# Kernel tuning notes

Hardware: AMD Instinct MI355X
Metric: run time of the kernel (lower is better)

Reference implementation:

```python
import jax, jax.numpy as jnp
import numpy as np

N, NUM_ST, NUM_LT = 8, 256, 4096
C_ST, C_LT, C_LAT = 512, 512, 128
LN_EPS = 1e-3  # keras LayerNormalization default epsilon


def setup_inputs() -> dict:
    key = jax.random.key(0)
    ks = jax.random.split(key, 12)
    w = lambda k, shape, sc=0.05: jax.random.normal(k, shape, jnp.float32) * sc
    return {
        "st_feat": jax.random.normal(ks[0], (N, NUM_ST, 1, 1, C_ST), jnp.float32),
        "lt_feat": jax.random.normal(ks[1], (N, NUM_LT, 1, 1, C_LT), jnp.float32),
        # conv1x1 kernels stored as (in, out) matrices
        "w_st": w(ks[2], (C_ST, C_LAT)),
        "b_st": w(ks[3], (C_LAT,), 0.01),
        "w_lt": w(ks[4], (C_LT, C_LAT)),
        "b_lt": w(ks[5], (C_LAT,), 0.01),
        "w_g": w(ks[6], (C_LT, C_LAT)),
        "b_g": w(ks[7], (C_LAT,), 0.01),
        # LayerNorm over axes [1,2,3,4] of (n, C_LAT, NUM_ST, 1, 1)
        "ln_gamma": 1.0 + w(ks[8], (C_LAT, NUM_ST, 1, 1), 0.02),
        "ln_beta": w(ks[9], (C_LAT, NUM_ST, 1, 1), 0.02),
        # out_conv: Conv3D on tensor with last dim 1 -> in_channels=1, kernel (out,)
        "w_out": w(ks[10], (C_ST,)),
        "b_out": w(ks[11], (C_ST,), 0.01),
    }


def reference(st_feat, lt_feat, w_st, b_st, w_lt, b_lt, w_g, b_g,
              ln_gamma, ln_beta, w_out, b_out):
    n = st_feat.shape[0]
    # 1x1x1 conv projections == matmul over last (channel) dim
    theta = jnp.einsum('nshwc,cd->nshwd', st_feat, w_st) + b_st  # (n,S,1,1,c)
    phi = jnp.einsum('nlhwc,cd->nlhwd', lt_feat, w_lt) + b_lt    # (n,L,1,1,c)
    g = jnp.einsum('nlhwc,cd->nlhwd', lt_feat, w_g) + b_g        # (n,L,1,1,c)
    # Faithful raw reshapes (row-major reinterpretation, as in the TF code)
    theta = theta.reshape(n, C_LAT, NUM_ST)
    phi = phi.reshape(n, C_LAT, NUM_LT)
    g = g.reshape(n, C_LAT, NUM_LT)
    # theta^T @ phi  -> (n, S, L)
    attn = jnp.einsum('ncs,ncl->nsl', theta, phi)
    attn = attn / jnp.sqrt(jnp.asarray(C_LAT, jnp.float32))  # use_scale
    p = jax.nn.softmax(attn, axis=-1)
    # g @ p^T -> (n, c, S)
    out = jnp.einsum('ncl,nsl->ncs', g, p)
    out = out.reshape(n, C_LAT, NUM_ST, 1, 1)
    # pre_activate: LayerNorm over all non-batch axes, then ReLU
    mean = jnp.mean(out, axis=(1, 2, 3, 4), keepdims=True)
    var = jnp.var(out, axis=(1, 2, 3, 4), keepdims=True)
    out = (out - mean) * jax.lax.rsqrt(var + LN_EPS) * ln_gamma + ln_beta
    out = jax.nn.relu(out)
    # out_conv: last dim is 1 -> broadcasts to C_ST output channels
    out = out * w_out + b_out  # (n, C_LAT, NUM_ST, 1, C_ST)
    # dropout is identity at inference
    return out
```

## Files before the change

### kernel.cpp

```cpp
#include <hip/hip_runtime.h>
#include <cstdint>

typedef unsigned short u16;
typedef unsigned int u32;
typedef __attribute__((ext_vector_type(8))) __bf16 bf16x8;
typedef __attribute__((ext_vector_type(4))) float f32x4;

__device__ __forceinline__ u32 f2bf_bits(float x) {
    u32 a = __builtin_bit_cast(u32, x);
    a += 0x7FFFu + ((a >> 16) & 1u);
    return a >> 16;
}
__device__ __forceinline__ u32 pack2(float lo, float hi) {
    u32 a = __builtin_bit_cast(u32, lo);
    u32 b = __builtin_bit_cast(u32, hi);
    a += 0x7FFFu + ((a >> 16) & 1u);
    b += 0x7FFFu + ((b >> 16) & 1u);
    return (a >> 16) | (b & 0xFFFF0000u);
}

#define LDS_STRIDE 72

__global__ void k0_wt(const float* __restrict__ w_lt, const float* __restrict__ w_g,
                      u16* __restrict__ wltT, u16* __restrict__ wgT) {
    int idx = blockIdx.x * 256 + threadIdx.x;
    int which = idx >> 16;
    int rem = idx & 65535;
    int nrow = rem >> 9;
    int k = rem & 511;
    const float* src = which ? w_g : w_lt;
    u16* dst = which ? wgT : wltT;
    dst[rem] = (u16)f2bf_bits(src[k * 128 + nrow]);
}

__global__ void k_init(float* __restrict__ stats) {
    if (threadIdx.x < 16) stats[threadIdx.x] = 0.f;
}

__global__ __launch_bounds__(256, 2) void k1_proj_lt(
    const float* __restrict__ lt,
    const u16* __restrict__ wltT, const u16* __restrict__ wgT,
    const float* __restrict__ b_lt, const float* __restrict__ b_g,
    u16* __restrict__ phi, u16* __restrict__ g)
{
    __shared__ u16 sA[128 * LDS_STRIDE];
    __shared__ u16 sBl[128 * LDS_STRIDE];
    __shared__ u16 sBg[128 * LDS_STRIDE];
    int tid = threadIdx.x;
    int wave = tid >> 6, lane = tid & 63, quad = lane >> 4, lq = lane & 15;
    int m0 = blockIdx.x * 128;
    int srow = tid >> 1, skc = (tid & 1) * 32;

    f32x4 zero = {0.f, 0.f, 0.f, 0.f};
    f32x4 acc[2][2][8];
    for (int p = 0; p < 2; p++)
        for (int mt = 0; mt < 2; mt++)
            for (int nt = 0; nt < 8; nt++) acc[p][mt][nt] = zero;

    for (int ko = 0; ko < 8; ko++) {
        {
            const float4* src = (const float4*)(lt + (size_t)(m0 + srow) * 512 + ko * 64 + skc);
            uint2* dst = (uint2*)&sA[srow * LDS_STRIDE + skc];
            #pragma unroll
            for (int i = 0; i < 8; i++) {
                float4 v = src[i];
                uint2 u; u.x = pack2(v.x, v.y); u.y = pack2(v.z, v.w);
                dst[i] = u;
            }
        }
        {
            const uint4* srcl = (const uint4*)(wltT + srow * 512 + ko * 64 + skc);
            const uint4* srcg = (const uint4*)(wgT  + srow * 512 + ko * 64 + skc);
            uint4* dstl = (uint4*)&sBl[srow * LDS_STRIDE + skc];
            uint4* dstg = (uint4*)&sBg[srow * LDS_STRIDE + skc];
            #pragma unroll
            for (int i = 0; i < 4; i++) { dstl[i] = srcl[i]; dstg[i] = srcg[i]; }
        }
        __syncthreads();
        #pragma unroll
        for (int kk = 0; kk < 2; kk++) {
            bf16x8 a[2], bl[8], bg[8];
            #pragma unroll
            for (int mt = 0; mt < 2; mt++)
                a[mt] = *(const bf16x8*)&sA[(wave * 32 + mt * 16 + lq) * LDS_STRIDE + kk * 32 + quad * 8];
            #pragma unroll
            for (int nt = 0; nt < 8; nt++) {
                bl[nt] = *(const bf16x8*)&sBl[(nt * 16 + lq) * LDS_STRIDE + kk * 32 + quad * 8];
                bg[nt] = *(const bf16x8*)&sBg[(nt * 16 + lq) * LDS_STRIDE + kk * 32 + quad * 8];
            }
            #pragma unroll
            for (int mt = 0; mt < 2; mt++)
                #pragma unroll
                for (int nt = 0; nt < 8; nt++) {
                    acc[0][mt][nt] = __builtin_amdgcn_mfma_f32_16x16x32_bf16(a[mt], bl[nt], acc[0][mt][nt], 0, 0, 0);
                    acc[1][mt][nt] = __builtin_amdgcn_mfma_f32_16x16x32_bf16(a[mt], bg[nt], acc[1][mt][nt], 0, 0, 0);
                }
        }
        __syncthreads();
    }
    #pragma unroll
    for (int mt = 0; mt < 2; mt++) {
        int mbase = m0 + wave * 32 + mt * 16 + quad * 4;
        #pragma unroll
        for (int nt = 0; nt < 8; nt++) {
            int n = nt * 16 + lq;
            float biasl = b_lt[n], biasg = b_g[n];
            #pragma unroll
            for (int r = 0; r < 4; r++) {
                size_t o = (size_t)(mbase + r) * 128 + n;
                phi[o] = (u16)f2bf_bits(acc[0][mt][nt][r] + biasl);
                g[o]   = (u16)f2bf_bits(acc[1][mt][nt][r] + biasg);
            }
        }
    }
}

__global__ __launch_bounds__(256) void k_tr(const u16* __restrict__ phi, u16* __restrict__ phiT)
{
    __shared__ u16 s[64 * 65];
    int bi = blockIdx.x;
    int n_idx = bi >> 7, rem = bi & 127;
    int c0 = (rem >> 6) * 64, l0 = (rem & 63) * 64;
    const u16* src = phi + (size_t)n_idx * 524288;
    u16* dst = phiT + (size_t)n_idx * 524288;
    int t = threadIdx.x;
    #pragma unroll
    for (int i = 0; i < 2; i++) {
        int idx = t + i * 256;
        int row = idx >> 3;
        int col = (idx & 7) * 8;
        uint4 v = *(const uint4*)(src + (size_t)(c0 + row) * 4096 + l0 + col);
        u16 tmp[8];
        *(uint4*)tmp = v;
        #pragma unroll
        for (int j = 0; j < 8; j++) s[row * 65 + col + j] = tmp[j];
    }
    __syncthreads();
    #pragma unroll
    for (int i = 0; i < 2; i++) {
        int idx = t + i * 256;
        int lrow = idx >> 3;
        int cb = (idx & 7) * 8;
        u16 tmp[8];
        #pragma unroll
        for (int j = 0; j < 8; j++) tmp[j] = s[(cb + j) * 65 + lrow];
        *(uint4*)(dst + (size_t)(l0 + lrow) * 128 + c0 + cb) = *(uint4*)tmp;
    }
}

__global__ __launch_bounds__(256) void k2_theta(
    const float* __restrict__ st, const float* __restrict__ w_st,
    const float* __restrict__ b_st, u16* __restrict__ thT)
{
    __shared__ float sA[8 * 512];
    int tid = threadIdx.x;
    int r0 = blockIdx.x * 8;
    {
        const float4* src = (const float4*)(st + (size_t)r0 * 512);
        float4* dst = (float4*)sA;
        #pragma unroll
        for (int i = 0; i < 4; i++) dst[tid + i * 256] = src[tid + i * 256];
    }
    __syncthreads();
    int d = tid & 127, rh = tid >> 7;
    float acc[4] = {0.f, 0.f, 0.f, 0.f};
    #pragma unroll 4
    for (int k = 0; k < 512; k++) {
        float w = w_st[(size_t)k * 128 + d];
        #pragma unroll
        for (int j = 0; j < 4; j++) acc[j] += sA[(rh + j * 2) * 512 + k] * w;
    }
    float bias = b_st[d];
    #pragma unroll
    for (int j = 0; j < 4; j++) {
        int r = r0 + rh + j * 2;
        int n_idx = r >> 8, s_raw = r & 255;
        int f = s_raw * 128 + d;
        thT[(size_t)n_idx * 32768 + (size_t)(f & 255) * 128 + (f >> 8)] =
            (u16)f2bf_bits(acc[j] + bias);
    }
}

__global__ __launch_bounds__(256, 2) void k3_attn(
    const u16* __restrict__ thT, const u16* __restrict__ phiT,
    float* __restrict__ attn)
{
    __shared__ u16 sA[128 * LDS_STRIDE];
    __shared__ u16 sB[128 * LDS_STRIDE];
    int tid = threadIdx.x;
    int wave = tid >> 6, lane = tid & 63, quad = lane >> 4, lq = lane & 15;
    int bi = blockIdx.x;
    int n_idx = bi >> 6, rem = bi & 63;
    int m0 = (rem >> 5) * 128;
    int l0 = (rem & 31) * 128;
    const u16* Ab = thT + (size_t)n_idx * 32768;
    const u16* Bb = phiT + (size_t)n_idx * 524288;
    int srow = tid >> 1, skc = (tid & 1) * 32;

    f32x4 zero = {0.f, 0.f, 0.f, 0.f};
    f32x4 acc[2][8];
    for (int mt = 0; mt < 2; mt++)
        for (int nt = 0; nt < 8; nt++) acc[mt][nt] = zero;

    for (int ko = 0; ko < 2; ko++) {
        const uint4* srcA = (const uint4*)(Ab + (size_t)(m0 + srow) * 128 + ko * 64 + skc);
        const uint4* srcB = (const uint4*)(Bb + (size_t)(l0 + srow) * 128 + ko * 64 + skc);
        uint4* dA = (uint4*)&sA[srow * LDS_STRIDE + skc];
        uint4* dB = (uint4*)&sB[srow * LDS_STRIDE + skc];
        #pragma unroll
        for (int i = 0; i < 4; i++) { dA[i] = srcA[i]; dB[i] = srcB[i]; }
        __syncthreads();
        #pragma unroll
        for (int kk = 0; kk < 2; kk++) {
            bf16x8 a[2], b[8];
            #pragma unroll
            for (int mt = 0; mt < 2; mt++)
                a[mt] = *(const bf16x8*)&sA[(wave * 32 + mt * 16 + lq) * LDS_STRIDE + kk * 32 + quad * 8];
            #pragma unroll
            for (int nt = 0; nt < 8; nt++)
                b[nt] = *(const bf16x8*)&sB[(nt * 16 + lq) * LDS_STRIDE + kk * 32 + quad * 8];
            #pragma unroll
            for (int mt = 0; mt < 2; mt++)
                #pragma unroll
                for (int nt = 0; nt < 8; nt++)
                    acc[mt][nt] = __builtin_amdgcn_mfma_f32_16x16x32_bf16(a[mt], b[nt], acc[mt][nt], 0, 0, 0);
        }
        __syncthreads();
    }
    const float scale = 0.08838834764831845f;
    float* Cb = attn + (size_t)n_idx * 1048576;
    #pragma unroll
    for (int mt = 0; mt < 2; mt++) {
        int mbase = m0 + wave * 32 + mt * 16 + quad * 4;
        #pragma unroll
        for (int nt = 0; nt < 8; nt++) {
            int col = l0 + nt * 16 + lq;
            #pragma unroll
            for (int r = 0; r < 4; r++)
                Cb[(size_t)(mbase + r) * 4096 + col] = acc[mt][nt][r] * scale;
        }
    }
}

__global__ __launch_bounds__(256) void k4_softmax(
    const float* __restrict__ attn, u16* __restrict__ p)
{
    __shared__ float red[256];
    int r = blockIdx.x;
    int tid = threadIdx.x;
    const float4* src = (const float4*)(attn + (size_t)r * 4096);
    float4 vv[4];
    float m = -1e30f;
    #pragma unroll
    for (int i = 0; i < 4; i++) {
        vv[i] = src[i * 256 + tid];
        m = fmaxf(m, fmaxf(fmaxf(vv[i].x, vv[i].y), fmaxf(vv[i].z, vv[i].w)));
    }
    red[tid] = m;
    __syncthreads();
    for (int s = 128; s > 0; s >>= 1) {
        if (tid < s) red[tid] = fmaxf(red[tid], red[tid + s]);
        __syncthreads();
    }
    m = red[0];
    __syncthreads();
    float sum = 0.f;
    #pragma unroll
    for (int i = 0; i < 4; i++) {
        vv[i].x = __expf(vv[i].x - m); vv[i].y = __expf(vv[i].y - m);
        vv[i].z = __expf(vv[i].z - m); vv[i].w = __expf(vv[i].w - m);
        sum += vv[i].x + vv[i].y + vv[i].z + vv[i].w;
    }
    red[tid] = sum;
    __syncthreads();
    for (int s = 128; s > 0; s >>= 1) {
        if (tid < s) red[tid] += red[tid + s];
        __syncthreads();
    }
    float inv = 1.0f / red[0];
    uint2* dst = (uint2*)(p + (size_t)r * 4096);
    #pragma unroll
    for (int i = 0; i < 4; i++) {
        uint2 u;
        u.x = pack2(vv[i].x * inv, vv[i].y * inv);
        u.y = pack2(vv[i].z * inv, vv[i].w * inv);
        dst[i * 256 + tid] = u;
    }
}

__global__ __launch_bounds__(256, 2) void k5_pv(
    const u16* __restrict__ g, const u16* __restrict__ p,
    float* __restrict__ opart)
{
    __shared__ u16 sA[128 * LDS_STRIDE];
    __shared__ u16 sB[128 * LDS_STRIDE];
    int tid = threadIdx.x;
    int wave = tid >> 6, lane = tid & 63, quad = lane >> 4, lq = lane & 15;
    int bi = blockIdx.x;
    int n_idx = bi >> 5, rem = bi & 31;
    int kch = rem >> 1, stile = rem & 1;
    int s0 = stile * 128;
    int l_base = kch * 256;
    const u16* Ab = g + (size_t)n_idx * 524288;
    const u16* Bb = p + (size_t)n_idx * 1048576;
    int srow = tid >> 1, skc = (tid & 1) * 32;

    f32x4 zero = {0.f, 0.f, 0.f, 0.f};
    f32x4 acc[2][8];
    for (int mt = 0; mt < 2; mt++)
        for (int nt = 0; nt < 8; nt++) acc[mt][nt] = zero;

    for (int ko = 0; ko < 4; ko++) {
        int l0 = l_base + ko * 64;
        const uint4* srcA = (const uint4*)(Ab + (size_t)srow * 4096 + l0 + skc);
        const uint4* srcB = (const uint4*)(Bb + (size_t)(s0 + srow) * 4096 + l0 + skc);
        uint4* dA = (uint4*)&sA[srow * LDS_STRIDE + skc];
        uint4* dB = (uint4*)&sB[srow * LDS_STRIDE + skc];
        #pragma unroll
        for (int i = 0; i < 4; i++) { dA[i] = srcA[i]; dB[i] = srcB[i]; }
        __syncthreads();
        #pragma unroll
        for (int kk = 0; kk < 2; kk++) {
            bf16x8 a[2], b[8];
            #pragma unroll
            for (int mt = 0; mt < 2; mt++)
                a[mt] = *(const bf16x8*)&sA[(wave * 32 + mt * 16 + lq) * LDS_STRIDE + kk * 32 + quad * 8];
            #pragma unroll
            for (int nt = 0; nt < 8; nt++)
                b[nt] = *(const bf16x8*)&sB[(nt * 16 + lq) * LDS_STRIDE + kk * 32 + quad * 8];
            #pragma unroll
            for (int mt = 0; mt < 2; mt++)
                #pragma unroll
                for (int nt = 0; nt < 8; nt++)
                    acc[mt][nt] = __builtin_amdgcn_mfma_f32_16x16x32_bf16(a[mt], b[nt], acc[mt][nt], 0, 0, 0);
        }
        __syncthreads();
    }
    float* Cb = opart + (size_t)(kch * 8 + n_idx) * 32768;
    #pragma unroll
    for (int mt = 0; mt < 2; mt++) {
        int cbase = wave * 32 + mt * 16 + quad * 4;
        #pragma unroll
        for (int nt = 0; nt < 8; nt++) {
            int s = s0 + nt * 16 + lq;
            #pragma unroll
            for (int r = 0; r < 4; r++)
                Cb[(size_t)(cbase + r) * 256 + s] = acc[mt][nt][r];
        }
    }
}

__global__ __launch_bounds__(256) void k5b_reduce(
    const float* __restrict__ opart, float* __restrict__ obuf,
    float* __restrict__ stats)
{
    __shared__ float red[256];
    __shared__ float red2[256];
    int tid = threadIdx.x;
    int bi = blockIdx.x;
    int n_idx = bi >> 4, part = bi & 15;
    int base = part * 2048;
    float lsum = 0.f, lsq = 0.f;
    for (int j = 0; j < 8; j++) {
        int idx = base + j * 256 + tid;
        float o = 0.f;
        #pragma unroll
        for (int ch = 0; ch < 16; ch++)
            o += opart[(size_t)(ch * 8 + n_idx) * 32768 + idx];
        obuf[(size_t)n_idx * 32768 + idx] = o;
        lsum += o; lsq += o * o;
    }
    red[tid] = lsum; red2[tid] = lsq;
    __syncthreads();
    for (int s = 128; s > 0; s >>= 1) {
        if (tid < s) { red[tid] += red[tid + s]; red2[tid] += red2[tid + s]; }
        __syncthreads();
    }
    if (tid == 0) {
        atomicAdd(&stats[n_idx * 2], red[0]);
        atomicAdd(&stats[n_idx * 2 + 1], red2[0]);
    }
}

__global__ __launch_bounds__(256) void k7_out(
    const float* __restrict__ obuf, const float* __restrict__ stats,
    const float* __restrict__ gamma, const float* __restrict__ beta,
    const float* __restrict__ w_out, const float* __restrict__ b_out,
    float4* __restrict__ out)
{
    long long idx4 = (long long)blockIdx.x * 256 + threadIdx.x;
    int row = (int)(idx4 >> 7);
    int k4 = (int)(idx4 & 127);
    int n_idx = row >> 15;
    int ridx = row & 32767;
    float o = obuf[row];
    float sum = stats[n_idx * 2], sq = stats[n_idx * 2 + 1];
    float mean = sum * (1.0f / 32768.0f);
    float var = sq * (1.0f / 32768.0f) - mean * mean;
    float rstd = rsqrtf(var + 1e-3f);
    float v = (o - mean) * rstd * gamma[ridx] + beta[ridx];
    v = fmaxf(v, 0.f);
    float4 w4 = ((const float4*)w_out)[k4];
    float4 b4 = ((const float4*)b_out)[k4];
    float4 r;
    r.x = fmaf(v, w4.x, b4.x);
    r.y = fmaf(v, w4.y, b4.y);
    r.z = fmaf(v, w4.z, b4.z);
    r.w = fmaf(v, w4.w, b4.w);
    out[idx4] = r;
}

extern "C" void kernel_launch(void* const* d_in, const int* in_sizes, int n_in,
                              void* d_out, int out_size, void* d_ws, size_t ws_size,
                              hipStream_t stream)
{
    (void)in_sizes; (void)n_in; (void)out_size; (void)ws_size;
    const float* st    = (const float*)d_in[0];
    const float* lt    = (const float*)d_in[1];
    const float* w_st  = (const float*)d_in[2];
    const float* b_st  = (const float*)d_in[3];
    const float* w_lt  = (const float*)d_in[4];
    const float* b_lt  = (const float*)d_in[5];
    const float* w_g   = (const float*)d_in[6];
    const float* b_g   = (const float*)d_in[7];
    const float* gamma = (const float*)d_in[8];
    const float* beta  = (const float*)d_in[9];
    const float* w_out = (const float*)d_in[10];
    const float* b_out = (const float*)d_in[11];

    char* ws = (char*)d_ws;
    u16*   phi   = (u16*)  (ws + 0);
    u16*   gbuf  = (u16*)  (ws + 8388608);
    u16*   thT   = (u16*)  (ws + 16777216);
    u16*   wltT  = (u16*)  (ws + 17301504);
    u16*   wgT   = (u16*)  (ws + 17432576);
    float* attn  = (float*)(ws + 17563648);
    u16*   pbuf  = (u16*)  (ws + 51118080);
    float* opart = (float*)(ws + 67895296);
    float* obuf  = (float*)(ws + 84672512);
    float* stats = (float*)(ws + 85721088);
    u16*   phiT  = (u16*)opart;

    k0_wt      <<<512,    256, 0, stream>>>(w_lt, w_g, wltT, wgT);
    k_init     <<<1,       64, 0, stream>>>(stats);
    k1_proj_lt <<<256,    256, 0, stream>>>(lt, wltT, wgT, b_lt, b_g, phi, gbuf);
    k_tr       <<<1024,   256, 0, stream>>>(phi, phiT);
    k2_theta   <<<256,    256, 0, stream>>>(st, w_st, b_st, thT);
    k3_attn    <<<512,    256, 0, stream>>>(thT, phiT, attn);
    k4_softmax <<<2048,   256, 0, stream>>>(attn, pbuf);
    k5_pv      <<<256,    256, 0, stream>>>(gbuf, pbuf, opart);
    k5b_reduce <<<128,    256, 0, stream>>>(opart, obuf, stats);
    k7_out     <<<131072, 256, 0, stream>>>(obuf, stats, gamma, beta, w_out, b_out,
                                            (float4*)d_out);
}
```

Before: 744.1 us.

## Fuse prep kernels, recompute softmax in PV load, widen output writes

Three small setup kernels (weight transpose, stats init, theta projection) are merged into one launch distinguished by block index. The softmax kernel now emits only per-row max and inverse sum. The PV kernel reads the fp32 scores and applies exp/normalize/bf16 pack while staging into LDS, which removes the bf16 probability buffer write and read but makes k5 read twice as many bytes and do exp work. The output kernel processes four float4s per thread with nontemporal stores to cut launch count and cache pollution on the large output write.

```diff
diff --git a/kernel.cpp b/kernel.cpp
--- a/kernel.cpp
+++ b/kernel.cpp
@@ -21,20 +21,56 @@
 
 #define LDS_STRIDE 72
 
-__global__ void k0_wt(const float* __restrict__ w_lt, const float* __restrict__ w_g,
-                      u16* __restrict__ wltT, u16* __restrict__ wgT) {
-    int idx = blockIdx.x * 256 + threadIdx.x;
-    int which = idx >> 16;
-    int rem = idx & 65535;
-    int nrow = rem >> 9;
-    int k = rem & 511;
-    const float* src = which ? w_g : w_lt;
-    u16* dst = which ? wgT : wltT;
-    dst[rem] = (u16)f2bf_bits(src[k * 128 + nrow]);
-}
-
-__global__ void k_init(float* __restrict__ stats) {
-    if (threadIdx.x < 16) stats[threadIdx.x] = 0.f;
+__global__ __launch_bounds__(256) void k_prep(
+    const float* __restrict__ w_lt, const float* __restrict__ w_g,
+    u16* __restrict__ wltT, u16* __restrict__ wgT,
+    const float* __restrict__ st, const float* __restrict__ w_st,
+    const float* __restrict__ b_st, u16* __restrict__ thT,
+    float* __restrict__ stats)
+{
+    __shared__ float sA[8 * 512];
+    int bi = blockIdx.x;
+    int tid = threadIdx.x;
+    if (bi < 512) {
+        int idx = bi * 256 + tid;
+        int which = idx >> 16;
+        int rem = idx & 65535;
+        int nrow = rem >> 9;
+        int k = rem & 511;
+        const float* src = which ? w_g : w_lt;
+        u16* dst = which ? wgT : wltT;
+        dst[rem] = (u16)f2bf_bits(src[k * 128 + nrow]);
+        return;
+    }
+    if (bi == 768) {
+        if (tid < 16) stats[tid] = 0.f;
+        return;
+    }
+    int r0 = (bi - 512) * 8;
+    {
+        const float4* src = (const float4*)(st + (size_t)r0 * 512);
+        float4* dst = (float4*)sA;
+        #pragma unroll
+        for (int i = 0; i < 4; i++) dst[tid + i * 256] = src[tid + i * 256];
+    }
+    __syncthreads();
+    int d = tid & 127, rh = tid >> 7;
+    float acc[4] = {0.f, 0.f, 0.f, 0.f};
+    #pragma unroll 4
+    for (int k = 0; k < 512; k++) {
+        float w = w_st[(size_t)k * 128 + d];
+        #pragma unroll
+        for (int j = 0; j < 4; j++) acc[j] += sA[(rh + j * 2) * 512 + k] * w;
+    }
+    float bias = b_st[d];
+    #pragma unroll
+    for (int j = 0; j < 4; j++) {
+        int r = r0 + rh + j * 2;
+        int n_idx = r >> 8, s_raw = r & 255;
+        int f = s_raw * 128 + d;
+        thT[(size_t)n_idx * 32768 + (size_t)(f & 255) * 128 + (f >> 8)] =
+            (u16)f2bf_bits(acc[j] + bias);
+    }
 }
 
 __global__ __launch_bounds__(256, 2) void k1_proj_lt(
@@ -145,39 +181,6 @@
         #pragma unroll
         for (int j = 0; j < 8; j++) tmp[j] = s[(cb + j) * 65 + lrow];
         *(uint4*)(dst + (size_t)(l0 + lrow) * 128 + c0 + cb) = *(uint4*)tmp;
-    }
-}
-
-__global__ __launch_bounds__(256) void k2_theta(
-    const float* __restrict__ st, const float* __restrict__ w_st,
-    const float* __restrict__ b_st, u16* __restrict__ thT)
-{
-    __shared__ float sA[8 * 512];
-    int tid = threadIdx.x;
-    int r0 = blockIdx.x * 8;
-    {
-        const float4* src = (const float4*)(st + (size_t)r0 * 512);
-        float4* dst = (float4*)sA;
-        #pragma unroll
-        for (int i = 0; i < 4; i++) dst[tid + i * 256] = src[tid + i * 256];
-    }
-    __syncthreads();
-    int d = tid & 127, rh = tid >> 7;
-    float acc[4] = {0.f, 0.f, 0.f, 0.f};
-    #pragma unroll 4
-    for (int k = 0; k < 512; k++) {
-        float w = w_st[(size_t)k * 128 + d];
-        #pragma unroll
-        for (int j = 0; j < 4; j++) acc[j] += sA[(rh + j * 2) * 512 + k] * w;
-    }
-    float bias = b_st[d];
-    #pragma unroll
-    for (int j = 0; j < 4; j++) {
-        int r = r0 + rh + j * 2;
-        int n_idx = r >> 8, s_raw = r & 255;
-        int f = s_raw * 128 + d;
-        thT[(size_t)n_idx * 32768 + (size_t)(f & 255) * 128 + (f >> 8)] =
-            (u16)f2bf_bits(acc[j] + bias);
     }
 }
 
@@ -242,8 +245,8 @@
     }
 }
 
-__global__ __launch_bounds__(256) void k4_softmax(
-    const float* __restrict__ attn, u16* __restrict__ p)
+__global__ __launch_bounds__(256) void k4_stats(
+    const float* __restrict__ attn, float* __restrict__ rowstat)
 {
     __shared__ float red[256];
     int r = blockIdx.x;
@@ -277,19 +280,15 @@
         if (tid < s) red[tid] += red[tid + s];
         __syncthreads();
     }
-    float inv = 1.0f / red[0];
-    uint2* dst = (uint2*)(p + (size_t)r * 4096);
-    #pragma unroll
-    for (int i = 0; i < 4; i++) {
-        uint2 u;
-        u.x = pack2(vv[i].x * inv, vv[i].y * inv);
-        u.y = pack2(vv[i].z * inv, vv[i].w * inv);
-        dst[i * 256 + tid] = u;
+    if (tid == 0) {
+        rowstat[r * 2]     = m;
+        rowstat[r * 2 + 1] = 1.0f / red[0];
     }
 }
 
 __global__ __launch_bounds__(256, 2) void k5_pv(
-    const u16* __restrict__ g, const u16* __restrict__ p,
+    const u16* __restrict__ g, const float* __restrict__ attn,
+    const float* __restrict__ rowstat,
     float* __restrict__ opart)
 {
     __shared__ u16 sA[128 * LDS_STRIDE];
@@ -302,8 +301,12 @@
     int s0 = stile * 128;
     int l_base = kch * 256;
     const u16* Ab = g + (size_t)n_idx * 524288;
-    const u16* Bb = p + (size_t)n_idx * 1048576;
     int srow = tid >> 1, skc = (tid & 1) * 32;
+
+    int sr_row = n_idx * 256 + s0 + srow;
+    float rm   = rowstat[sr_row * 2];
+    float rinv = rowstat[sr_row * 2 + 1];
+    const float* Brow = attn + (size_t)sr_row * 4096;
 
     f32x4 zero = {0.f, 0.f, 0.f, 0.f};
     f32x4 acc[2][8];
@@ -313,11 +316,19 @@
     for (int ko = 0; ko < 4; ko++) {
         int l0 = l_base + ko * 64;
         const uint4* srcA = (const uint4*)(Ab + (size_t)srow * 4096 + l0 + skc);
-        const uint4* srcB = (const uint4*)(Bb + (size_t)(s0 + srow) * 4096 + l0 + skc);
+        const float4* srcB = (const float4*)(Brow + l0 + skc);
         uint4* dA = (uint4*)&sA[srow * LDS_STRIDE + skc];
-        uint4* dB = (uint4*)&sB[srow * LDS_STRIDE + skc];
-        #pragma unroll
-        for (int i = 0; i < 4; i++) { dA[i] = srcA[i]; dB[i] = srcB[i]; }
+        uint2* dB = (uint2*)&sB[srow * LDS_STRIDE + skc];
+        #pragma unroll
+        for (int i = 0; i < 4; i++) dA[i] = srcA[i];
+        #pragma unroll
+        for (int i = 0; i < 8; i++) {
+            float4 v = srcB[i];
+            uint2 u;
+            u.x = pack2(__expf(v.x - rm) * rinv, __expf(v.y - rm) * rinv);
+            u.y = pack2(__expf(v.z - rm) * rinv, __expf(v.w - rm) * rinv);
+            dB[i] = u;
+        }
         __syncthreads();
         #pragma unroll
         for (int kk = 0; kk < 2; kk++) {
@@ -386,28 +397,36 @@
     const float* __restrict__ obuf, const float* __restrict__ stats,
     const float* __restrict__ gamma, const float* __restrict__ beta,
     const float* __restrict__ w_out, const float* __restrict__ b_out,
-    float4* __restrict__ out)
-{
-    long long idx4 = (long long)blockIdx.x * 256 + threadIdx.x;
-    int row = (int)(idx4 >> 7);
-    int k4 = (int)(idx4 & 127);
-    int n_idx = row >> 15;
-    int ridx = row & 32767;
-    float o = obuf[row];
+    float* __restrict__ out)
+{
+    int tid = threadIdx.x;
+    long long base = (long long)blockIdx.x * 1024;
+    int r0 = blockIdx.x * 8 + (tid >> 7);
+    int k4i = tid & 127;
+    int n_idx = r0 >> 15;
     float sum = stats[n_idx * 2], sq = stats[n_idx * 2 + 1];
     float mean = sum * (1.0f / 32768.0f);
     float var = sq * (1.0f / 32768.0f) - mean * mean;
     float rstd = rsqrtf(var + 1e-3f);
-    float v = (o - mean) * rstd * gamma[ridx] + beta[ridx];
-    v = fmaxf(v, 0.f);
-    float4 w4 = ((const float4*)w_out)[k4];
-    float4 b4 = ((const float4*)b_out)[k4];
-    float4 r;
-    r.x = fmaf(v, w4.x, b4.x);
-    r.y = fmaf(v, w4.y, b4.y);
-    r.z = fmaf(v, w4.z, b4.z);
-    r.w = fmaf(v, w4.w, b4.w);
-    out[idx4] = r;
+    const f32x4* w4p = (const f32x4*)w_out;
+    const f32x4* b4p = (const f32x4*)b_out;
+    f32x4 w4 = w4p[k4i];
+    f32x4 b4 = b4p[k4i];
+    f32x4* out4 = (f32x4*)out;
+    #pragma unroll
+    for (int i = 0; i < 4; i++) {
+        int row = r0 + i * 2;
+        int ridx = row & 32767;
+        float o = obuf[row];
+        float v = (o - mean) * rstd * gamma[ridx] + beta[ridx];
+        v = fmaxf(v, 0.f);
+        f32x4 r;
+        r.x = __builtin_fmaf(v, w4.x, b4.x);
+        r.y = __builtin_fmaf(v, w4.y, b4.y);
+        r.z = __builtin_fmaf(v, w4.z, b4.z);
+        r.w = __builtin_fmaf(v, w4.w, b4.w);
+        __builtin_nontemporal_store(r, &out4[base + tid + i * 256]);
+    }
 }
 
 extern "C" void kernel_launch(void* const* d_in, const int* in_sizes, int n_in,
@@ -429,27 +448,25 @@
     const float* b_out = (const float*)d_in[11];
 
     char* ws = (char*)d_ws;
-    u16*   phi   = (u16*)  (ws + 0);
-    u16*   gbuf  = (u16*)  (ws + 8388608);
-    u16*   thT   = (u16*)  (ws + 16777216);
-    u16*   wltT  = (u16*)  (ws + 17301504);
-    u16*   wgT   = (u16*)  (ws + 17432576);
-    float* attn  = (float*)(ws + 17563648);
-    u16*   pbuf  = (u16*)  (ws + 51118080);
-    float* opart = (float*)(ws + 67895296);
-    float* obuf  = (float*)(ws + 84672512);
-    float* stats = (float*)(ws + 85721088);
-    u16*   phiT  = (u16*)opart;
-
-    k0_wt      <<<512,    256, 0, stream>>>(w_lt, w_g, wltT, wgT);
-    k_init     <<<1,       64, 0, stream>>>(stats);
-    k1_proj_lt <<<256,    256, 0, stream>>>(lt, wltT, wgT, b_lt, b_g, phi, gbuf);
-    k_tr       <<<1024,   256, 0, stream>>>(phi, phiT);
-    k2_theta   <<<256,    256, 0, stream>>>(st, w_st, b_st, thT);
-    k3_attn    <<<512,    256, 0, stream>>>(thT, phiT, attn);
-    k4_softmax <<<2048,   256, 0, stream>>>(attn, pbuf);
-    k5_pv      <<<256,    256, 0, stream>>>(gbuf, pbuf, opart);
-    k5b_reduce <<<128,    256, 0, stream>>>(opart, obuf, stats);
-    k7_out     <<<131072, 256, 0, stream>>>(obuf, stats, gamma, beta, w_out, b_out,
-                                            (float4*)d_out);
-}
+    u16*   phi    = (u16*)  (ws + 0);
+    u16*   gbuf   = (u16*)  (ws + 8388608);
+    u16*   thT    = (u16*)  (ws + 16777216);
+    u16*   wltT   = (u16*)  (ws + 17301504);
+    u16*   wgT    = (u16*)  (ws + 17432576);
+    float* attn   = (float*)(ws + 17563648);
+    float* rowstat= (float*)(ws + 51118080);
+    float* opart  = (float*)(ws + 67895296);
+    float* obuf   = (float*)(ws + 84672512);
+    float* stats  = (float*)(ws + 85721088);
+    u16*   phiT   = (u16*)opart;
+
+    k_prep     <<<769,   256, 0, stream>>>(w_lt, w_g, wltT, wgT, st, w_st, b_st, thT, stats);
+    k1_proj_lt <<<256,   256, 0, stream>>>(lt, wltT, wgT, b_lt, b_g, phi, gbuf);
+    k_tr       <<<1024,  256, 0, stream>>>(phi, phiT);
+    k3_attn    <<<512,   256, 0, stream>>>(thT, phiT, attn);
+    k4_stats   <<<2048,  256, 0, stream>>>(attn, rowstat);
+    k5_pv      <<<256,   256, 0, stream>>>(gbuf, attn, rowstat, opart);
+    k5b_reduce <<<128,   256, 0, stream>>>(opart, obuf, stats);
+    k7_out     <<<32768, 256, 0, stream>>>(obuf, stats, gamma, beta, w_out, b_out,
+                                           (float*)d_out);
+}
```

After: 702.2 us. 1.06x faster.
